# Kernel tuning notes

Measured on AMD Instinct MI355X. Metric: run time of the kernel, lower is better.

The kernel has to match this reference:

```python
import jax, jax.numpy as jnp
import numpy as np

N, E, B, IN, DIM, H = 20000, 320000, 128, 25, 64, 8

def _lin(key, fin, fout):
    k1, k2 = jax.random.split(key)
    s = 1.0 / np.sqrt(fin)
    return (jax.random.uniform(k1, (fin, fout), jnp.float32, -s, s),
            jax.random.uniform(k2, (fout,), jnp.float32, -s, s))

def setup_inputs() -> dict:
    key = jax.random.key(0)
    ks = jax.random.split(key, 12)
    x = jax.random.normal(ks[0], (N, IN), jnp.float32)
    edge_index = jax.random.randint(ks[1], (2, E), 0, N, jnp.int64)
    batch = jnp.sort(jax.random.randint(ks[2], (N,), 0, B, jnp.int64))
    W0, b0 = _lin(ks[3], IN, DIM)
    Wg, _ = _lin(ks[4], DIM, H * DIM)            # GATConv lin (no bias)
    att_src = jax.random.normal(ks[5], (H, DIM), jnp.float32) * (1.0 / np.sqrt(DIM))
    att_dst = jax.random.normal(ks[6], (H, DIM), jnp.float32) * (1.0 / np.sqrt(DIM))
    bg = jnp.zeros((H * DIM,), jnp.float32)       # GATConv output bias
    Wh, bh = _lin(ks[7], H * DIM, DIM)            # head_nn
    sl = 1.0 / np.sqrt(DIM)
    W_ih = jax.random.uniform(ks[8], (4 * DIM, 2 * DIM), jnp.float32, -sl, sl)
    W_hh = jax.random.uniform(ks[9], (4 * DIM, DIM), jnp.float32, -sl, sl)
    b_ih = jnp.zeros((4 * DIM,), jnp.float32)
    b_hh = jnp.zeros((4 * DIM,), jnp.float32)
    W1, b1 = _lin(ks[10], 2 * DIM, DIM)
    W2, b2 = _lin(ks[11], DIM, 1)
    return dict(x=x, edge_index=edge_index, batch=batch, W0=W0, b0=b0, Wg=Wg,
                att_src=att_src, att_dst=att_dst, bg=bg, Wh=Wh, bh=bh,
                W_ih=W_ih, W_hh=W_hh, b_ih=b_ih, b_hh=b_hh, W1=W1, b1=b1, W2=W2, b2=b2)

def _forward(x, edge_index, batch, W0, b0, Wg, att_src, att_dst, bg, Wh, bh,
             W_ih, W_hh, b_ih, b_hh, W1, b1, W2, b2):
    n = x.shape[0]
    h0 = jax.nn.relu(x @ W0 + b0)                         # [N, DIM]
    xh = (h0 @ Wg).reshape(n, H, DIM)                     # [N, H, C]
    # add self-loops (PyG GATConv default)
    loop = jnp.arange(n, dtype=edge_index.dtype)
    src = jnp.concatenate([edge_index[0], loop])
    dst = jnp.concatenate([edge_index[1], loop])
    a_s = jnp.einsum('nhc,hc->nh', xh, att_src)           # [N, H]
    a_d = jnp.einsum('nhc,hc->nh', xh, att_dst)
    e = jax.nn.leaky_relu(a_s[src] + a_d[dst], 0.2)       # [Etot, H]
    m = jax.ops.segment_max(e, dst, num_segments=n)
    w = jnp.exp(e - m[dst])
    s = jax.ops.segment_sum(w, dst, num_segments=n)
    alpha = w / s[dst]                                    # segment softmax over dst
    agg = jax.ops.segment_sum(alpha[:, :, None] * xh[src], dst, num_segments=n)
    out = jax.nn.relu(agg.reshape(n, H * DIM) + bg)
    out = jax.nn.relu(out @ Wh + bh)                      # [N, DIM]
    # Set2Set, 3 processing steps
    q_star = jnp.zeros((B, 2 * DIM), out.dtype)
    h = jnp.zeros((B, DIM), out.dtype)
    c = jnp.zeros((B, DIM), out.dtype)
    for _ in range(3):
        g = q_star @ W_ih.T + b_ih + h @ W_hh.T + b_hh
        i_g, f_g, g_g, o_g = jnp.split(g, 4, axis=-1)
        c = jax.nn.sigmoid(f_g) * c + jax.nn.sigmoid(i_g) * jnp.tanh(g_g)
        h = jax.nn.sigmoid(o_g) * jnp.tanh(c)
        q = h                                             # [B, DIM]
        e2 = jnp.sum(out * q[batch], axis=-1)             # [N]
        m2 = jax.ops.segment_max(e2, batch, num_segments=B)
        w2 = jnp.exp(e2 - m2[batch])
        s2 = jax.ops.segment_sum(w2, batch, num_segments=B)
        a2 = w2 / s2[batch]
        r = jax.ops.segment_sum(a2[:, None] * out, batch, num_segments=B)
        q_star = jnp.concatenate([q, r], axis=-1)
    y = jax.nn.relu(q_star @ W1 + b1)
    y = y @ W2 + b2
    return y.reshape(-1)

def reference(x, edge_index, batch, W0, b0, Wg, att_src, att_dst, bg, Wh, bh,
              W_ih, W_hh, b_ih, b_hh, W1, b1, W2, b2):
    return _forward(x, edge_index, batch, W0, b0, Wg, att_src, att_dst, bg, Wh, bh,
                    W_ih, W_hh, b_ih, b_hh, W1, b1, W2, b2)
```

## Files before the change

kernel.cpp:

```cpp
#include <hip/hip_runtime.h>

#define N_NODES 20000
#define N_EDGES 320000
#define NBATCH  128

__device__ __forceinline__ float lrelu(float v) { return v > 0.f ? v : 0.2f * v; }
__device__ __forceinline__ float rdlane(float v, int l) {
    return __int_as_float(__builtin_amdgcn_readlane(__float_as_int(v), l));
}

__global__ void k_small(const float* __restrict__ Wg, const float* __restrict__ att_s,
                        const float* __restrict__ att_d, float* __restrict__ vsd,
                        const int* __restrict__ batch, int* __restrict__ segst,
                        int* __restrict__ deg, int n, int b) {
    int tid = threadIdx.x;
    int gid = blockIdx.x * 256 + tid;
    if (gid < n) deg[gid] = 0;
    if (blockIdx.x < 2) {
        int t = blockIdx.x * 256 + tid;
        int k = t >> 3, h = t & 7;
        const float* wrow = Wg + (size_t)k * 512 + h * 64;
        float s1 = 0.f, s2 = 0.f;
        #pragma unroll 8
        for (int c = 0; c < 64; c++) {
            float w = wrow[c];
            s1 += w * att_s[h * 64 + c];
            s2 += w * att_d[h * 64 + c];
        }
        vsd[k * 16 + h] = s1;
        vsd[k * 16 + 8 + h] = s2;
    } else if (blockIdx.x == 2) {
        if (tid > b) return;
        int lo = 0, hi = n;
        while (lo < hi) { int mid = (lo + hi) >> 1; if (batch[mid] < tid) lo = mid + 1; else hi = mid; }
        segst[tid] = lo;
    }
}

__global__ void k_h0c(const float* __restrict__ x, const float* __restrict__ W0,
                      const float* __restrict__ b0, float* __restrict__ h0,
                      const int* __restrict__ edst, int* __restrict__ deg, int n) {
    __shared__ float ws[25 * 64];
    __shared__ float bs[64];
    __shared__ float xs[100];
    int t = threadIdx.x;
    if (t < 64) {
        int e = blockIdx.x * 64 + t;
        atomicAdd(&deg[edst[e]], 1);
    }
    for (int i = t; i < 25 * 64; i += 256) ws[i] = W0[i];
    if (t < 64) bs[t] = b0[t];
    int nb = blockIdx.x * 4;
    if (t < 100 && nb * 25 + t < n * 25) xs[t] = x[(size_t)nb * 25 + t];
    __syncthreads();
    int node = nb + (t >> 6);
    int c = t & 63;
    if (node >= n) return;
    float s = bs[c];
    const float* xr = xs + (t >> 6) * 25;
    #pragma unroll
    for (int k = 0; k < 25; k++) s += xr[k] * ws[k * 64 + c];
    h0[(size_t)node * 64 + c] = fmaxf(s, 0.f);
}

__global__ __launch_bounds__(256) void k_asd_scan(const float* __restrict__ h0,
                                                  const float* __restrict__ vsd,
                                                  float* __restrict__ a_s, float* __restrict__ a_d,
                                                  const int* __restrict__ deg,
                                                  int* __restrict__ tmp, int* __restrict__ bsum,
                                                  int nasd, int n) {
    __shared__ float hs[16][65];
    __shared__ float vl[64 * 16];
    __shared__ int wsum[4];
    int tid = threadIdx.x;
    if (blockIdx.x >= nasd) {
        int s = blockIdx.x - nasd;
        int i = s * 256 + tid;
        int lane = tid & 63, w = tid >> 6;
        int v = (i < n) ? deg[i] + 1 : 0;
        int x = v;
        #pragma unroll
        for (int off = 1; off < 64; off <<= 1) {
            int t2 = __shfl_up(x, off);
            if (lane >= off) x += t2;
        }
        if (lane == 63) wsum[w] = x;
        __syncthreads();
        int pre = 0;
        #pragma unroll
        for (int j = 0; j < 4; j++) if (j < w) pre += wsum[j];
        if (i < n) tmp[i] = pre + x - v;
        if (tid == 255) bsum[s] = pre + x;
        return;
    }
    int rbase = blockIdx.x * 16;
    {
        int row = tid / 16, c4 = (tid % 16) * 4;
        float4 hv = *(const float4*)(h0 + (size_t)(rbase + row) * 64 + c4);
        hs[row][c4] = hv.x; hs[row][c4 + 1] = hv.y; hs[row][c4 + 2] = hv.z; hs[row][c4 + 3] = hv.w;
    }
    #pragma unroll
    for (int j = 0; j < 4; j++) vl[tid + j * 256] = vsd[tid + j * 256];
    __syncthreads();
    int nl = tid / 16, o = tid % 16;
    float acc = 0.f;
    #pragma unroll 16
    for (int k = 0; k < 64; k++) acc += hs[nl][k] * vl[k * 16 + o];
    int node = rbase + nl;
    if (o < 8) a_s[node * 8 + o] = acc;
    else       a_d[node * 8 + (o - 8)] = acc;
}

__global__ void k_scan2(const int* __restrict__ tmp, const int* __restrict__ bsum,
                        int* __restrict__ offs, int* __restrict__ adj,
                        int* __restrict__ cursor, int n, int nblk) {
    int i = blockIdx.x * 256 + threadIdx.x;
    if (i > n) return;
    int b = i >> 8;
    int pre = 0;
    for (int j = 0; j < b; j++) pre += bsum[j];
    if (i == n) {
        int tot = pre;
        for (int j = b; j < nblk; j++) tot += bsum[j];
        offs[n] = tot;
        return;
    }
    int o = pre + tmp[i];
    offs[i] = o;
    adj[o] = i;
    cursor[i] = o + 1;
}

__global__ void k_fill_edge(const int* __restrict__ src, const int* __restrict__ dst,
                            int* __restrict__ cursor, int* __restrict__ adj, int e) {
    int i = blockIdx.x * 256 + threadIdx.x;
    if (i >= e) return;
    int p = atomicAdd(&cursor[dst[i]], 1);
    adj[p] = src[i];
}

__global__ __launch_bounds__(256) void k_gat6(const int* __restrict__ offs, const int* __restrict__ adj,
                                              const float* __restrict__ a_s, const float* __restrict__ a_d,
                                              const float* __restrict__ h0,
                                              float* __restrict__ agg_pre, int n) {
    int lane = threadIdx.x & 63;
    int node = blockIdx.x * 4 + (threadIdx.x >> 6);
    if (node >= n) return;
    int beg = offs[node], end = offs[node + 1];
    int g = lane >> 3, h = lane & 7;
    float ad = a_d[node * 8 + h];

    float m = -1e30f, s = 0.f;
    for (int i = beg + g; i < end; i += 8) {
        int src = adj[i];
        float e = lrelu(a_s[src * 8 + h] + ad);
        if (e > m) { s = s * __expf(m - e) + 1.f; m = e; }
        else       { s += __expf(e - m); }
    }
    #pragma unroll
    for (int off = 8; off < 64; off <<= 1) {
        float mo = __shfl_xor(m, off), so = __shfl_xor(s, off);
        float mn = fmaxf(m, mo);
        s = s * __expf(m - mn) + so * __expf(mo - mn);
        m = mn;
    }
    float rcp = 1.f / s;

    float acc[8] = {0.f, 0.f, 0.f, 0.f, 0.f, 0.f, 0.f, 0.f};
    for (int sbase = beg; sbase < end; sbase += 64) {
        int scnt = end - sbase; if (scnt > 64) scnt = 64;
        int srcv = 0;
        if (lane < scnt) srcv = adj[sbase + lane];
        float al[8];
        #pragma unroll
        for (int j = 0; j < 8; j++) {
            int q = j * 8 + g;
            float alv = 0.f;
            if (q < scnt) {
                int sq = __shfl(srcv, q);
                float e = lrelu(a_s[sq * 8 + h] + ad);
                alv = __expf(e - m) * rcp;
            }
            al[j] = alv;
        }
        #pragma unroll
        for (int j = 0; j < 8; j += 2) {
            int qb0 = j * 8, qb1 = (j + 1) * 8;
            if (qb0 >= scnt) break;
            bool has1 = qb1 < scnt;
            int sg0[8], sg1[8];
            float xv0[8], xv1[8];
            #pragma unroll
            for (int g2 = 0; g2 < 8; g2++) sg0[g2] = __builtin_amdgcn_readlane(srcv, qb0 + g2);
            #pragma unroll
            for (int g2 = 0; g2 < 8; g2++) sg1[g2] = __builtin_amdgcn_readlane(srcv, qb1 + g2);
            #pragma unroll
            for (int g2 = 0; g2 < 8; g2++) xv0[g2] = h0[(size_t)sg0[g2] * 64 + lane];
            if (has1) {
                #pragma unroll
                for (int g2 = 0; g2 < 8; g2++) xv1[g2] = h0[(size_t)sg1[g2] * 64 + lane];
            }
            #pragma unroll
            for (int g2 = 0; g2 < 8; g2++) {
                #pragma unroll
                for (int h2 = 0; h2 < 8; h2++)
                    acc[h2] += rdlane(al[j], g2 * 8 + h2) * xv0[g2];
            }
            if (has1) {
                #pragma unroll
                for (int g2 = 0; g2 < 8; g2++) {
                    #pragma unroll
                    for (int h2 = 0; h2 < 8; h2++)
                        acc[h2] += rdlane(al[j + 1], g2 * 8 + h2) * xv1[g2];
                }
            }
        }
    }
    #pragma unroll
    for (int h2 = 0; h2 < 8; h2++)
        agg_pre[(size_t)node * 512 + h2 * 64 + lane] = acc[h2];
}

__global__ __launch_bounds__(256) void k_fused4(const float* __restrict__ agg_pre,
                                                const float* __restrict__ Wg,
                                                const float* __restrict__ bg,
                                                const float* __restrict__ Wh,
                                                float* __restrict__ part, int M) {
    __shared__ float AB[64 * 68];
    __shared__ float Bs[64 * 64];
    int tid = threadIdx.x;
    int r0 = blockIdx.x * 64;
    int tx = tid & 7;
    int ty = tid >> 3;
    int rr = tid >> 4, c4 = (tid & 15) * 4;
    float4 accO[2][2] = {};
    #pragma unroll
    for (int hh = 0; hh < 2; hh++) {
        int h = blockIdx.y * 2 + hh;
        #pragma unroll
        for (int pp = 0; pp < 4; pp++) {
            int r = rr + pp * 16;
            float4 av = make_float4(0.f, 0.f, 0.f, 0.f);
            if (r0 + r < M) av = *(const float4*)(agg_pre + (size_t)(r0 + r) * 512 + h * 64 + c4);
            *(float4*)&AB[r * 68 + c4] = av;
            *(float4*)&Bs[r * 64 + c4] = *(const float4*)(Wg + (size_t)r * 512 + h * 64 + c4);
        }
        __syncthreads();
        float4 acc1[2][2] = {};
        #pragma unroll 4
        for (int kc = 0; kc < 16; kc++) {
            float4 a0 = *(const float4*)&AB[(ty * 2 + 0) * 68 + kc * 4];
            float4 a1 = *(const float4*)&AB[(ty * 2 + 1) * 68 + kc * 4];
            #pragma unroll
            for (int kk = 0; kk < 4; kk++) {
                float ak0 = (&a0.x)[kk], ak1 = (&a1.x)[kk];
                float4 bL = *(const float4*)&Bs[(kc * 4 + kk) * 64 + tx * 8];
                float4 bH = *(const float4*)&Bs[(kc * 4 + kk) * 64 + tx * 8 + 4];
                acc1[0][0].x += ak0 * bL.x; acc1[0][0].y += ak0 * bL.y; acc1[0][0].z += ak0 * bL.z; acc1[0][0].w += ak0 * bL.w;
                acc1[0][1].x += ak0 * bH.x; acc1[0][1].y += ak0 * bH.y; acc1[0][1].z += ak0 * bH.z; acc1[0][1].w += ak0 * bH.w;
                acc1[1][0].x += ak1 * bL.x; acc1[1][0].y += ak1 * bL.y; acc1[1][0].z += ak1 * bL.z; acc1[1][0].w += ak1 * bL.w;
                acc1[1][1].x += ak1 * bH.x; acc1[1][1].y += ak1 * bH.y; acc1[1][1].z += ak1 * bH.z; acc1[1][1].w += ak1 * bH.w;
            }
        }
        __syncthreads();
        float4 bgL = *(const float4*)(bg + h * 64 + tx * 8);
        float4 bgH = *(const float4*)(bg + h * 64 + tx * 8 + 4);
        #pragma unroll
        for (int i = 0; i < 2; i++) {
            float4 cL, cH;
            cL.x = fmaxf(acc1[i][0].x + bgL.x, 0.f); cL.y = fmaxf(acc1[i][0].y + bgL.y, 0.f);
            cL.z = fmaxf(acc1[i][0].z + bgL.z, 0.f); cL.w = fmaxf(acc1[i][0].w + bgL.w, 0.f);
            cH.x = fmaxf(acc1[i][1].x + bgH.x, 0.f); cH.y = fmaxf(acc1[i][1].y + bgH.y, 0.f);
            cH.z = fmaxf(acc1[i][1].z + bgH.z, 0.f); cH.w = fmaxf(acc1[i][1].w + bgH.w, 0.f);
            *(float4*)&AB[(ty * 2 + i) * 68 + tx * 8] = cL;
            *(float4*)&AB[(ty * 2 + i) * 68 + tx * 8 + 4] = cH;
        }
        #pragma unroll
        for (int pp = 0; pp < 4; pp++) {
            int k = rr + pp * 16;
            *(float4*)&Bs[k * 64 + c4] = *(const float4*)(Wh + (size_t)(h * 64 + k) * 64 + c4);
        }
        __syncthreads();
        #pragma unroll 4
        for (int kc = 0; kc < 16; kc++) {
            float4 a0 = *(const float4*)&AB[(ty * 2 + 0) * 68 + kc * 4];
            float4 a1 = *(const float4*)&AB[(ty * 2 + 1) * 68 + kc * 4];
            #pragma unroll
            for (int kk = 0; kk < 4; kk++) {
                float ak0 = (&a0.x)[kk], ak1 = (&a1.x)[kk];
                float4 bL = *(const float4*)&Bs[(kc * 4 + kk) * 64 + tx * 8];
                float4 bH = *(const float4*)&Bs[(kc * 4 + kk) * 64 + tx * 8 + 4];
                accO[0][0].x += ak0 * bL.x; accO[0][0].y += ak0 * bL.y; accO[0][0].z += ak0 * bL.z; accO[0][0].w += ak0 * bL.w;
                accO[0][1].x += ak0 * bH.x; accO[0][1].y += ak0 * bH.y; accO[0][1].z += ak0 * bH.z; accO[0][1].w += ak0 * bH.w;
                accO[1][0].x += ak1 * bL.x; accO[1][0].y += ak1 * bL.y; accO[1][0].z += ak1 * bL.z; accO[1][0].w += ak1 * bL.w;
                accO[1][1].x += ak1 * bH.x; accO[1][1].y += ak1 * bH.y; accO[1][1].z += ak1 * bH.z; accO[1][1].w += ak1 * bH.w;
            }
        }
        __syncthreads();
    }
    float* Cb = part + (size_t)blockIdx.y * M * 64;
    #pragma unroll
    for (int i = 0; i < 2; i++) {
        int r = r0 + ty * 2 + i;
        if (r >= M) continue;
        *(float4*)(Cb + (size_t)r * 64 + tx * 8) = accO[i][0];
        *(float4*)(Cb + (size_t)r * 64 + tx * 8 + 4) = accO[i][1];
    }
}

#define SROWS 208
__global__ __launch_bounds__(256) void k_s2s(const float* __restrict__ part,
                                             const float* __restrict__ bh,
                                             const int* __restrict__ segst,
                                             const float* __restrict__ W_ih, const float* __restrict__ W_hh,
                                             const float* __restrict__ b_ih, const float* __restrict__ b_hh,
                                             const float* __restrict__ W1, const float* __restrict__ b1,
                                             const float* __restrict__ W2, const float* __restrict__ b2,
                                             float* __restrict__ out, int M) {
    int b = blockIdx.x, tid = threadIdx.x, lane = tid & 63, w = tid >> 6;
    __shared__ float sc[SROWS * 65];
    __shared__ float wlds[1024];
    __shared__ float hl[64], cl[64], rl_[64];
    __shared__ float red[4];
    __shared__ float gsh[256];
    int beg = segst[b], end = segst[b + 1];
    int nrows = end - beg;
    int ncache = nrows < SROWS ? nrows : SROWS;
    const size_t PS = (size_t)M * 64;
    for (int idx = tid; idx < ncache * 16; idx += 256) {
        int r = idx >> 4, q = idx & 15;
        const float* pb = part + (size_t)(beg + r) * 64 + q * 4;
        float4 v0 = *(const float4*)pb;
        float4 v1 = *(const float4*)(pb + PS);
        float4 v2 = *(const float4*)(pb + 2 * PS);
        float4 v3 = *(const float4*)(pb + 3 * PS);
        float4 bv = *(const float4*)(bh + q * 4);
        float* p = &sc[r * 65 + q * 4];
        p[0] = fmaxf(v0.x + v1.x + v2.x + v3.x + bv.x, 0.f);
        p[1] = fmaxf(v0.y + v1.y + v2.y + v3.y + bv.y, 0.f);
        p[2] = fmaxf(v0.z + v1.z + v2.z + v3.z + bv.z, 0.f);
        p[3] = fmaxf(v0.w + v1.w + v2.w + v3.w + bv.w, 0.f);
    }
    if (tid < 64) { hl[tid] = 0.f; cl[tid] = 0.f; rl_[tid] = 0.f; }
    __syncthreads();

    for (int it = 0; it < 3; it++) {
        {
            float acc = b_ih[tid] + b_hh[tid];
            const float* wi = W_ih + (size_t)tid * 128;
            const float* wh = W_hh + (size_t)tid * 64;
            #pragma unroll 8
            for (int k = 0; k < 64; k++) acc += hl[k] * (wi[k] + wh[k]) + rl_[k] * wi[64 + k];
            gsh[tid] = acc;
        }
        __syncthreads();
        if (tid < 64) {
            float ig = gsh[tid], fg = gsh[64 + tid], gg = gsh[128 + tid], og = gsh[192 + tid];
            float cc = cl[tid];
            float si = 1.f / (1.f + __expf(-ig));
            float sf = 1.f / (1.f + __expf(-fg));
            float so = 1.f / (1.f + __expf(-og));
            float cn = sf * cc + si * tanhf(gg);
            cl[tid] = cn;
            hl[tid] = so * tanhf(cn);
        }
        __syncthreads();
        float ev[4];
        int nr = 0;
        float mloc = -1e30f;
        for (int i = tid; i < nrows; i += 256) {
            float d = 0.f;
            if (i < SROWS) {
                const float* rp = &sc[i * 65];
                #pragma unroll 16
                for (int j = 0; j < 64; j++) d += rp[j] * hl[j];
            } else {
                const float* pb = part + (size_t)(beg + i) * 64;
                for (int j = 0; j < 64; j++) {
                    float v = pb[j] + pb[PS + j] + pb[2 * PS + j] + pb[3 * PS + j] + bh[j];
                    d += fmaxf(v, 0.f) * hl[j];
                }
            }
            ev[nr++] = d;
            mloc = fmaxf(mloc, d);
        }
        #pragma unroll
        for (int off = 1; off < 64; off <<= 1) mloc = fmaxf(mloc, __shfl_xor(mloc, off));
        if (lane == 0) red[w] = mloc;
        __syncthreads();
        float m = fmaxf(fmaxf(red[0], red[1]), fmaxf(red[2], red[3]));
        __syncthreads();
        float sloc = 0.f;
        nr = 0;
        for (int i = tid; i < nrows; i += 256) {
            float wv = __expf(ev[nr++] - m);
            if (i < 1024) wlds[i] = wv;
            sloc += wv;
        }
        #pragma unroll
        for (int off = 1; off < 64; off <<= 1) sloc += __shfl_xor(sloc, off);
        if (lane == 0) red[w] = sloc;
        __syncthreads();
        float sv = red[0] + red[1] + red[2] + red[3];
        float inv = sv > 0.f ? 1.f / sv : 0.f;
        float acc = 0.f;
        for (int i = w; i < nrows; i += 4) {
            float v;
            if (i < SROWS) v = sc[i * 65 + lane];
            else {
                const float* pb = part + (size_t)(beg + i) * 64 + lane;
                v = fmaxf(pb[0] + pb[PS] + pb[2 * PS] + pb[3 * PS] + bh[lane], 0.f);
            }
            acc += wlds[i] * v;
        }
        gsh[w * 64 + lane] = acc;
        __syncthreads();
        if (tid < 64)
            rl_[tid] = (gsh[tid] + gsh[64 + tid] + gsh[128 + tid] + gsh[192 + tid]) * inv;
        __syncthreads();
    }
    if (tid < 64) {
        float t = b1[tid];
        #pragma unroll 8
        for (int k = 0; k < 64; k++)
            t += hl[k] * W1[(size_t)k * 64 + tid] + rl_[k] * W1[(size_t)(64 + k) * 64 + tid];
        t = fmaxf(t, 0.f) * W2[tid];
        #pragma unroll
        for (int off = 32; off > 0; off >>= 1) t += __shfl_xor(t, off);
        if (tid == 0) out[b] = t + b2[0];
    }
}

extern "C" void kernel_launch(void* const* d_in, const int* in_sizes, int n_in,
                              void* d_out, int out_size, void* d_ws, size_t ws_size,
                              hipStream_t stream) {
    const float* x     = (const float*)d_in[0];
    const int*   ei    = (const int*)d_in[1];
    const int*   batch = (const int*)d_in[2];
    const float* W0    = (const float*)d_in[3];
    const float* b0    = (const float*)d_in[4];
    const float* Wg    = (const float*)d_in[5];
    const float* att_s = (const float*)d_in[6];
    const float* att_d = (const float*)d_in[7];
    const float* bg    = (const float*)d_in[8];
    const float* Wh    = (const float*)d_in[9];
    const float* bh    = (const float*)d_in[10];
    const float* W_ih  = (const float*)d_in[11];
    const float* W_hh  = (const float*)d_in[12];
    const float* b_ih  = (const float*)d_in[13];
    const float* b_hh  = (const float*)d_in[14];
    const float* W1    = (const float*)d_in[15];
    const float* b1    = (const float*)d_in[16];
    const float* W2    = (const float*)d_in[17];
    const float* b2    = (const float*)d_in[18];
    float* out = (float*)d_out;

    const int* esrc = ei;
    const int* edst = ei + N_EDGES;

    char* wsb = (char*)d_ws;
    size_t off = 0;
    auto alloc = [&](size_t bytes) {
        void* p = wsb + off;
        off = (off + bytes + 255) & ~(size_t)255;
        return p;
    };
    float* h0      = (float*)alloc((size_t)N_NODES * 64 * 4);
    float* agg_pre = (float*)alloc((size_t)N_NODES * 512 * 4);
    float* part    = (float*)alloc((size_t)4 * N_NODES * 64 * 4);
    float* a_s     = (float*)alloc((size_t)N_NODES * 8 * 4);
    float* a_d     = (float*)alloc((size_t)N_NODES * 8 * 4);
    float* vsd     = (float*)alloc(64 * 16 * 4);
    int*   deg     = (int*)alloc((size_t)N_NODES * 4);
    int*   tmp     = (int*)alloc((size_t)N_NODES * 4);
    int*   bsum    = (int*)alloc(128 * 4);
    int*   offs    = (int*)alloc((size_t)(N_NODES + 1) * 4);
    int*   cursor  = (int*)alloc((size_t)N_NODES * 4);
    int*   adj     = (int*)alloc((size_t)(N_EDGES + N_NODES) * 4);
    int*   segst   = (int*)alloc((size_t)(NBATCH + 1) * 4);

    const int nscan = (N_NODES + 255) / 256;
    const int nasd  = N_NODES / 16;

    k_small<<<82, 256, 0, stream>>>(Wg, att_s, att_d, vsd, batch, segst, deg, N_NODES, NBATCH);
    k_h0c<<<N_NODES / 4, 256, 0, stream>>>(x, W0, b0, h0, edst, deg, N_NODES);
    k_asd_scan<<<nasd + nscan, 256, 0, stream>>>(h0, vsd, a_s, a_d, deg, tmp, bsum, nasd, N_NODES);

    k_scan2<<<(N_NODES + 256) / 256, 256, 0, stream>>>(tmp, bsum, offs, adj, cursor, N_NODES, nscan);
    k_fill_edge<<<(N_EDGES + 255) / 256, 256, 0, stream>>>(esrc, edst, cursor, adj, N_EDGES);

    k_gat6<<<(N_NODES + 3) / 4, 256, 0, stream>>>(offs, adj, a_s, a_d, h0, agg_pre, N_NODES);
    k_fused4<<<dim3((N_NODES + 63) / 64, 4), 256, 0, stream>>>(agg_pre, Wg, bg, Wh, part, N_NODES);

    k_s2s<<<NBATCH, 256, 0, stream>>>(part, bh, segst, W_ih, W_hh, b_ih, b_hh, W1, b1, W2, b2, out, N_NODES);
}
```

Before: 260.6 us.

## Replace FP32 SIMT fused GEMMs with split-bf16 MFMA kernel

The fused per-head GEMM pair (agg_pre·Wg then ReLU then ·Wh) moves from FP32 FMA tiling in shared memory to MFMA 16x16x32 bf16 instructions. A split hi/lo bf16 (three-product) scheme keeps accuracy close to FP32. Wg and Wh are pre-split and transposed into bf16 hi/lo buffers by extra blocks in the setup kernel. The new kernel uses single-wave 64-thread blocks over 16-row tiles and reads the weight fragments straight from global memory or cache. That trades LDS reuse for more global weight traffic and extra conversion work.

```diff
diff --git a/kernel.cpp b/kernel.cpp
--- a/kernel.cpp
+++ b/kernel.cpp
@@ -4,15 +4,28 @@
 #define N_EDGES 320000
 #define NBATCH  128
 
+typedef __attribute__((ext_vector_type(8))) short s8v;
+typedef __attribute__((ext_vector_type(4))) float f32x4;
+typedef __attribute__((ext_vector_type(4))) int i32x4;
+
 __device__ __forceinline__ float lrelu(float v) { return v > 0.f ? v : 0.2f * v; }
 __device__ __forceinline__ float rdlane(float v, int l) {
     return __int_as_float(__builtin_amdgcn_readlane(__float_as_int(v), l));
 }
-
-__global__ void k_small(const float* __restrict__ Wg, const float* __restrict__ att_s,
-                        const float* __restrict__ att_d, float* __restrict__ vsd,
+__device__ __forceinline__ unsigned short bf16_rne(float f) {
+    unsigned u = __float_as_uint(f);
+    unsigned r = u + 0x7FFF + ((u >> 16) & 1);
+    return (unsigned short)(r >> 16);
+}
+
+__global__ void k_small(const float* __restrict__ Wg, const float* __restrict__ Wh,
+                        const float* __restrict__ att_s, const float* __restrict__ att_d,
+                        float* __restrict__ vsd,
                         const int* __restrict__ batch, int* __restrict__ segst,
-                        int* __restrict__ deg, int n, int b) {
+                        int* __restrict__ deg,
+                        unsigned short* __restrict__ wgt_hi, unsigned short* __restrict__ wgt_lo,
+                        unsigned short* __restrict__ wht_hi, unsigned short* __restrict__ wht_lo,
+                        int n, int b) {
     int tid = threadIdx.x;
     int gid = blockIdx.x * 256 + tid;
     if (gid < n) deg[gid] = 0;
@@ -34,6 +47,19 @@
         int lo = 0, hi = n;
         while (lo < hi) { int mid = (lo + hi) >> 1; if (batch[mid] < tid) lo = mid + 1; else hi = mid; }
         segst[tid] = lo;
+    } else {
+        int wi = (blockIdx.x - 3) * 256 + tid;
+        int sel = wi >> 15;
+        int r = wi & 32767;
+        int h = r >> 12, nn = (r >> 6) & 63, k = r & 63;
+        float val = (sel == 0) ? Wg[(size_t)k * 512 + h * 64 + nn]
+                               : Wh[(size_t)(h * 64 + k) * 64 + nn];
+        unsigned short hi = bf16_rne(val);
+        float hf = __uint_as_float((unsigned)hi << 16);
+        unsigned short lo = bf16_rne(val - hf);
+        int o = h * 4096 + nn * 64 + k;
+        if (sel == 0) { wgt_hi[o] = hi; wgt_lo[o] = lo; }
+        else          { wht_hi[o] = hi; wht_lo[o] = lo; }
     }
 }
 
@@ -221,90 +247,101 @@
         agg_pre[(size_t)node * 512 + h2 * 64 + lane] = acc[h2];
 }
 
-__global__ __launch_bounds__(256) void k_fused4(const float* __restrict__ agg_pre,
-                                                const float* __restrict__ Wg,
-                                                const float* __restrict__ bg,
-                                                const float* __restrict__ Wh,
-                                                float* __restrict__ part, int M) {
-    __shared__ float AB[64 * 68];
-    __shared__ float Bs[64 * 64];
-    int tid = threadIdx.x;
-    int r0 = blockIdx.x * 64;
-    int tx = tid & 7;
-    int ty = tid >> 3;
-    int rr = tid >> 4, c4 = (tid & 15) * 4;
-    float4 accO[2][2] = {};
+__global__ __launch_bounds__(64) void k_fmma(const float* __restrict__ agg_pre,
+                                             const unsigned short* __restrict__ wgt_hi,
+                                             const unsigned short* __restrict__ wgt_lo,
+                                             const unsigned short* __restrict__ wht_hi,
+                                             const unsigned short* __restrict__ wht_lo,
+                                             const float* __restrict__ bg,
+                                             float* __restrict__ part, int M) {
+    __shared__ unsigned C1[16 * 68];
+    int lane = threadIdx.x;
+    int m = lane & 15, quad = lane >> 4;
+    int r0 = blockIdx.x * 16;
+    int pair = blockIdx.y;
+    f32x4 accO[4];
+    #pragma unroll
+    for (int i = 0; i < 4; i++) accO[i] = (f32x4){0.f, 0.f, 0.f, 0.f};
+
     #pragma unroll
     for (int hh = 0; hh < 2; hh++) {
-        int h = blockIdx.y * 2 + hh;
-        #pragma unroll
-        for (int pp = 0; pp < 4; pp++) {
-            int r = rr + pp * 16;
-            float4 av = make_float4(0.f, 0.f, 0.f, 0.f);
-            if (r0 + r < M) av = *(const float4*)(agg_pre + (size_t)(r0 + r) * 512 + h * 64 + c4);
-            *(float4*)&AB[r * 68 + c4] = av;
-            *(float4*)&Bs[r * 64 + c4] = *(const float4*)(Wg + (size_t)r * 512 + h * 64 + c4);
-        }
-        __syncthreads();
-        float4 acc1[2][2] = {};
-        #pragma unroll 4
-        for (int kc = 0; kc < 16; kc++) {
-            float4 a0 = *(const float4*)&AB[(ty * 2 + 0) * 68 + kc * 4];
-            float4 a1 = *(const float4*)&AB[(ty * 2 + 1) * 68 + kc * 4];
-            #pragma unroll
-            for (int kk = 0; kk < 4; kk++) {
-                float ak0 = (&a0.x)[kk], ak1 = (&a1.x)[kk];
-                float4 bL = *(const float4*)&Bs[(kc * 4 + kk) * 64 + tx * 8];
-                float4 bH = *(const float4*)&Bs[(kc * 4 + kk) * 64 + tx * 8 + 4];
-                acc1[0][0].x += ak0 * bL.x; acc1[0][0].y += ak0 * bL.y; acc1[0][0].z += ak0 * bL.z; acc1[0][0].w += ak0 * bL.w;
-                acc1[0][1].x += ak0 * bH.x; acc1[0][1].y += ak0 * bH.y; acc1[0][1].z += ak0 * bH.z; acc1[0][1].w += ak0 * bH.w;
-                acc1[1][0].x += ak1 * bL.x; acc1[1][0].y += ak1 * bL.y; acc1[1][0].z += ak1 * bL.z; acc1[1][0].w += ak1 * bL.w;
-                acc1[1][1].x += ak1 * bH.x; acc1[1][1].y += ak1 * bH.y; acc1[1][1].z += ak1 * bH.z; acc1[1][1].w += ak1 * bH.w;
-            }
-        }
-        __syncthreads();
-        float4 bgL = *(const float4*)(bg + h * 64 + tx * 8);
-        float4 bgH = *(const float4*)(bg + h * 64 + tx * 8 + 4);
-        #pragma unroll
-        for (int i = 0; i < 2; i++) {
-            float4 cL, cH;
-            cL.x = fmaxf(acc1[i][0].x + bgL.x, 0.f); cL.y = fmaxf(acc1[i][0].y + bgL.y, 0.f);
-            cL.z = fmaxf(acc1[i][0].z + bgL.z, 0.f); cL.w = fmaxf(acc1[i][0].w + bgL.w, 0.f);
-            cH.x = fmaxf(acc1[i][1].x + bgH.x, 0.f); cH.y = fmaxf(acc1[i][1].y + bgH.y, 0.f);
-            cH.z = fmaxf(acc1[i][1].z + bgH.z, 0.f); cH.w = fmaxf(acc1[i][1].w + bgH.w, 0.f);
-            *(float4*)&AB[(ty * 2 + i) * 68 + tx * 8] = cL;
-            *(float4*)&AB[(ty * 2 + i) * 68 + tx * 8 + 4] = cH;
-        }
-        #pragma unroll
-        for (int pp = 0; pp < 4; pp++) {
-            int k = rr + pp * 16;
-            *(float4*)&Bs[k * 64 + c4] = *(const float4*)(Wh + (size_t)(h * 64 + k) * 64 + c4);
-        }
-        __syncthreads();
-        #pragma unroll 4
-        for (int kc = 0; kc < 16; kc++) {
-            float4 a0 = *(const float4*)&AB[(ty * 2 + 0) * 68 + kc * 4];
-            float4 a1 = *(const float4*)&AB[(ty * 2 + 1) * 68 + kc * 4];
-            #pragma unroll
-            for (int kk = 0; kk < 4; kk++) {
-                float ak0 = (&a0.x)[kk], ak1 = (&a1.x)[kk];
-                float4 bL = *(const float4*)&Bs[(kc * 4 + kk) * 64 + tx * 8];
-                float4 bH = *(const float4*)&Bs[(kc * 4 + kk) * 64 + tx * 8 + 4];
-                accO[0][0].x += ak0 * bL.x; accO[0][0].y += ak0 * bL.y; accO[0][0].z += ak0 * bL.z; accO[0][0].w += ak0 * bL.w;
-                accO[0][1].x += ak0 * bH.x; accO[0][1].y += ak0 * bH.y; accO[0][1].z += ak0 * bH.z; accO[0][1].w += ak0 * bH.w;
-                accO[1][0].x += ak1 * bL.x; accO[1][0].y += ak1 * bL.y; accO[1][0].z += ak1 * bL.z; accO[1][0].w += ak1 * bL.w;
-                accO[1][1].x += ak1 * bH.x; accO[1][1].y += ak1 * bH.y; accO[1][1].z += ak1 * bH.z; accO[1][1].w += ak1 * bH.w;
-            }
-        }
-        __syncthreads();
-    }
-    float* Cb = part + (size_t)blockIdx.y * M * 64;
-    #pragma unroll
-    for (int i = 0; i < 2; i++) {
-        int r = r0 + ty * 2 + i;
-        if (r >= M) continue;
-        *(float4*)(Cb + (size_t)r * 64 + tx * 8) = accO[i][0];
-        *(float4*)(Cb + (size_t)r * 64 + tx * 8 + 4) = accO[i][1];
+        int h = pair * 2 + hh;
+        s8v ahi[2], alo[2];
+        #pragma unroll
+        for (int ks = 0; ks < 2; ks++) {
+            const float* ap = agg_pre + (size_t)(r0 + m) * 512 + h * 64 + ks * 32 + quad * 8;
+            float av[8];
+            *(float4*)&av[0] = *(const float4*)ap;
+            *(float4*)&av[4] = *(const float4*)(ap + 4);
+            #pragma unroll
+            for (int j = 0; j < 8; j++) {
+                unsigned short hi = bf16_rne(av[j]);
+                float hf = __uint_as_float((unsigned)hi << 16);
+                unsigned short lo = bf16_rne(av[j] - hf);
+                ahi[ks][j] = (short)hi;
+                alo[ks][j] = (short)lo;
+            }
+        }
+        #pragma unroll
+        for (int tn = 0; tn < 4; tn++) {
+            f32x4 acc = (f32x4){0.f, 0.f, 0.f, 0.f};
+            #pragma unroll
+            for (int ks = 0; ks < 2; ks++) {
+                const unsigned short* bp = wgt_hi + h * 4096 + (tn * 16 + m) * 64 + ks * 32 + quad * 8;
+                const unsigned short* bl = wgt_lo + h * 4096 + (tn * 16 + m) * 64 + ks * 32 + quad * 8;
+                s8v bhf = *(const s8v*)bp;
+                s8v blf = *(const s8v*)bl;
+                acc = __builtin_amdgcn_mfma_f32_16x16x32_bf16(alo[ks], bhf, acc, 0, 0, 0);
+                acc = __builtin_amdgcn_mfma_f32_16x16x32_bf16(ahi[ks], blf, acc, 0, 0, 0);
+                acc = __builtin_amdgcn_mfma_f32_16x16x32_bf16(ahi[ks], bhf, acc, 0, 0, 0);
+            }
+            float bgv = bg[h * 64 + tn * 16 + m];
+            #pragma unroll
+            for (int r = 0; r < 4; r++) {
+                float v = fmaxf(acc[r] + bgv, 0.f);
+                unsigned short hi = bf16_rne(v);
+                float hf = __uint_as_float((unsigned)hi << 16);
+                unsigned short lo = bf16_rne(v - hf);
+                C1[(quad * 4 + r) * 68 + tn * 16 + m] = (unsigned)hi | ((unsigned)lo << 16);
+            }
+        }
+        __syncthreads();
+        s8v a2h[2], a2l[2];
+        #pragma unroll
+        for (int ks = 0; ks < 2; ks++) {
+            const unsigned* cp = &C1[m * 68 + ks * 32 + quad * 8];
+            unsigned uu[8];
+            *(i32x4*)&uu[0] = *(const i32x4*)cp;
+            *(i32x4*)&uu[4] = *(const i32x4*)(cp + 4);
+            #pragma unroll
+            for (int j = 0; j < 8; j++) {
+                a2h[ks][j] = (short)(uu[j] & 0xFFFFu);
+                a2l[ks][j] = (short)(uu[j] >> 16);
+            }
+        }
+        #pragma unroll
+        for (int tn = 0; tn < 4; tn++) {
+            #pragma unroll
+            for (int ks = 0; ks < 2; ks++) {
+                const unsigned short* bp = wht_hi + h * 4096 + (tn * 16 + m) * 64 + ks * 32 + quad * 8;
+                const unsigned short* bl = wht_lo + h * 4096 + (tn * 16 + m) * 64 + ks * 32 + quad * 8;
+                s8v bhf = *(const s8v*)bp;
+                s8v blf = *(const s8v*)bl;
+                accO[tn] = __builtin_amdgcn_mfma_f32_16x16x32_bf16(a2l[ks], bhf, accO[tn], 0, 0, 0);
+                accO[tn] = __builtin_amdgcn_mfma_f32_16x16x32_bf16(a2h[ks], blf, accO[tn], 0, 0, 0);
+                accO[tn] = __builtin_amdgcn_mfma_f32_16x16x32_bf16(a2h[ks], bhf, accO[tn], 0, 0, 0);
+            }
+        }
+        __syncthreads();
+    }
+    float* Cb = part + (size_t)pair * M * 64;
+    #pragma unroll
+    for (int tn = 0; tn < 4; tn++) {
+        #pragma unroll
+        for (int r = 0; r < 4; r++) {
+            int row = r0 + quad * 4 + r;
+            Cb[(size_t)row * 64 + tn * 16 + m] = accO[tn][r];
+        }
     }
 }
 
@@ -471,6 +508,10 @@
     float* a_s     = (float*)alloc((size_t)N_NODES * 8 * 4);
     float* a_d     = (float*)alloc((size_t)N_NODES * 8 * 4);
     float* vsd     = (float*)alloc(64 * 16 * 4);
+    unsigned short* wgt_hi = (unsigned short*)alloc(32768 * 2);
+    unsigned short* wgt_lo = (unsigned short*)alloc(32768 * 2);
+    unsigned short* wht_hi = (unsigned short*)alloc(32768 * 2);
+    unsigned short* wht_lo = (unsigned short*)alloc(32768 * 2);
     int*   deg     = (int*)alloc((size_t)N_NODES * 4);
     int*   tmp     = (int*)alloc((size_t)N_NODES * 4);
     int*   bsum    = (int*)alloc(128 * 4);
@@ -482,7 +523,8 @@
     const int nscan = (N_NODES + 255) / 256;
     const int nasd  = N_NODES / 16;
 
-    k_small<<<82, 256, 0, stream>>>(Wg, att_s, att_d, vsd, batch, segst, deg, N_NODES, NBATCH);
+    k_small<<<259, 256, 0, stream>>>(Wg, Wh, att_s, att_d, vsd, batch, segst, deg,
+                                     wgt_hi, wgt_lo, wht_hi, wht_lo, N_NODES, NBATCH);
     k_h0c<<<N_NODES / 4, 256, 0, stream>>>(x, W0, b0, h0, edst, deg, N_NODES);
     k_asd_scan<<<nasd + nscan, 256, 0, stream>>>(h0, vsd, a_s, a_d, deg, tmp, bsum, nasd, N_NODES);
 
@@ -490,7 +532,8 @@
     k_fill_edge<<<(N_EDGES + 255) / 256, 256, 0, stream>>>(esrc, edst, cursor, adj, N_EDGES);
 
     k_gat6<<<(N_NODES + 3) / 4, 256, 0, stream>>>(offs, adj, a_s, a_d, h0, agg_pre, N_NODES);
-    k_fused4<<<dim3((N_NODES + 63) / 64, 4), 256, 0, stream>>>(agg_pre, Wg, bg, Wh, part, N_NODES);
+    k_fmma<<<dim3(N_NODES / 16, 4), 64, 0, stream>>>(agg_pre, wgt_hi, wgt_lo, wht_hi, wht_lo,
+                                                     bg, part, N_NODES);
 
     k_s2s<<<NBATCH, 256, 0, stream>>>(part, bh, segst, W_ih, W_hh, b_ih, b_hh, W1, b1, W2, b2, out, N_NODES);
 }
```

Measured after the change: 267.0 us. 2.4% more time.
